# Kernel optimization log

Measured on AMD Instinct MI355X. Metric: run time of the kernel, lower is better.

Reference implementation:

```python
import jax, jax.numpy as jnp
import numpy as np

B, H = 16384, 1024  # batch, hidden (= input_size; module requires equality)


def _glorot(k, shape):
    lim = 1.0 / np.sqrt(shape[-1])
    return jax.random.uniform(k, shape, jnp.float32, -lim, lim)


def setup_inputs() -> dict:
    key = jax.random.key(0)
    ks = jax.random.split(key, 20)
    inp = {
        "d_t": jax.random.normal(ks[0], (B, H), jnp.float32),
        "h_t_minus_1": jax.random.normal(ks[1], (B, H), jnp.float32),
        "c_t_minus_1": jax.random.normal(ks[2], (B, H), jnp.float32),
    }
    names = ["i", "f", "o", "c", "g"]
    for n, (ka, kb, kc) in zip(names, zip(ks[3:8], ks[8:13], ks[13:18])):
        inp[f"W_{n}"] = _glorot(ka, (H, H))  # Linear weight [out,in], has bias
        inp[f"b_{n}"] = _glorot(kb, (H,))
        inp[f"U_{n}"] = _glorot(kc, (H, H))  # Linear weight, no bias
    return inp


def reference(d_t, h_t_minus_1, c_t_minus_1,
              W_i, b_i, U_i, W_f, b_f, U_f, W_o, b_o, U_o,
              W_c, b_c, U_c, W_g, b_g, U_g):
    def lin2(W, b, U):  # W(d) + U(h)
        return d_t @ W.T + b + h_t_minus_1 @ U.T

    i_t = jax.nn.sigmoid(lin2(W_i, b_i, U_i))
    f_t = jax.nn.sigmoid(lin2(W_f, b_f, U_f))
    o_t = jax.nn.sigmoid(lin2(W_o, b_o, U_o))
    c_hat_t = jnp.tanh(lin2(W_c, b_c, U_c))
    g_t = jax.nn.sigmoid(lin2(W_g, b_g, U_g))

    c_t = i_t * c_hat_t + f_t * c_t_minus_1
    # per-row dot products (original uses bmm on [B,1,H]x[B,H,1])
    num = jnp.sum(c_t * c_t_minus_1, axis=-1, keepdims=True)      # [B,1]
    den = jnp.sum(c_t_minus_1 * c_t_minus_1, axis=-1, keepdims=True)
    fraction = num / den                                           # [B,1] broadcast to [B,H]
    c_div_t = c_t - g_t * fraction * c_t_minus_1
    h_t = o_t * jnp.tanh(c_div_t)
    return (h_t, c_t)
```

## Files before the change

kernel.cpp:

```cpp
#include <hip/hip_runtime.h>
#include <hip/hip_bf16.h>

#define B_ROWS 16384
#define HDIM   1024
#define KDIM   2048
#define NDIM   5120

typedef __attribute__((ext_vector_type(8))) __bf16 bf16x8;
typedef __attribute__((ext_vector_type(4))) float  f32x4;

#define WS_OFF_B    67108864UL
#define WS_OFF_BIAS 88080384UL
#define WS_OFF_P    88100864UL

__device__ __forceinline__ void async16(const void* g, void* l) {
  __builtin_amdgcn_global_load_lds(
      (__attribute__((address_space(1))) void*)(g),
      (__attribute__((address_space(3))) void*)(l), 16, 0, 0);
}

__device__ __forceinline__ float fast_sigmoid(float x) {
  return 1.0f / (1.0f + __expf(-x));
}
__device__ __forceinline__ float fast_tanh(float x) {
  return 1.0f - 2.0f / (__expf(2.0f * x) + 1.0f);
}

struct GatePtrs {
  const float* W[5];
  const float* U[5];
  const float* b[5];
};

__global__ __launch_bounds__(256) void pack_A(const float* __restrict__ d,
                                              const float* __restrict__ h,
                                              __bf16* __restrict__ A) {
  const int idx = blockIdx.x * 256 + threadIdx.x;
  const size_t flat = (size_t)idx * 8;
  const int r = (int)(flat >> 11);
  const int c = (int)(flat & 2047);
  const float* src = (c < HDIM) ? (d + (size_t)r * HDIM + c)
                                : (h + (size_t)r * HDIM + (c - HDIM));
  const float4 v0 = ((const float4*)src)[0];
  const float4 v1 = ((const float4*)src)[1];
  bf16x8 o;
  o[0] = (__bf16)v0.x; o[1] = (__bf16)v0.y; o[2] = (__bf16)v0.z; o[3] = (__bf16)v0.w;
  o[4] = (__bf16)v1.x; o[5] = (__bf16)v1.y; o[6] = (__bf16)v1.z; o[7] = (__bf16)v1.w;
  *(bf16x8*)(A + flat) = o;
}

__global__ __launch_bounds__(256) void pack_B(GatePtrs gp, __bf16* __restrict__ Bm) {
  const int idx = blockIdx.x * 256 + threadIdx.x;
  const size_t flat = (size_t)idx * 8;
  const int row = (int)(flat >> 11);
  const int c = (int)(flat & 2047);
  const int g = row >> 10;
  const int oo = row & 1023;
  const float* base = (c < HDIM) ? gp.W[g] : gp.U[g];
  const float* src = base + (size_t)oo * HDIM + (c & 1023);
  const float4 v0 = ((const float4*)src)[0];
  const float4 v1 = ((const float4*)src)[1];
  bf16x8 o;
  o[0] = (__bf16)v0.x; o[1] = (__bf16)v0.y; o[2] = (__bf16)v0.z; o[3] = (__bf16)v0.w;
  o[4] = (__bf16)v1.x; o[5] = (__bf16)v1.y; o[6] = (__bf16)v1.z; o[7] = (__bf16)v1.w;
  *(bf16x8*)(Bm + flat) = o;
}

__global__ __launch_bounds__(256) void pack_bias(GatePtrs gp, float* __restrict__ bias) {
  const int i = blockIdx.x * 256 + threadIdx.x;
  bias[i] = gp.b[i >> 10][i & 1023];
}

__global__ __launch_bounds__(256) void gemm_act(const __bf16* __restrict__ A,
                                                const __bf16* __restrict__ Bm,
                                                const float* __restrict__ bias,
                                                __bf16* __restrict__ P) {
  __shared__ __align__(16) __bf16 As[128 * 64];
  __shared__ __align__(16) __bf16 Bs[128 * 64];

  const int tid  = threadIdx.x;
  const int lane = tid & 63;
  const int wave = tid >> 6;
  const int quad = lane >> 4;
  const int lr   = lane & 15;
  const int sx   = lr & 7;
  const int wm   = (wave >> 1) << 6;
  const int wn   = (wave & 1) << 6;

  const int row0 = blockIdx.x * 128;
  const int col0 = blockIdx.y * 128;

  f32x4 acc[4][4] = {};

  for (int kt = 0; kt < KDIM; kt += 64) {
#pragma unroll
    for (int t = 0; t < 4; ++t) {
      const int c  = t * 256 + tid;
      const int r  = c >> 3;
      const int q  = (c & 7) ^ (r & 7);
      async16(A  + (size_t)(row0 + r) * KDIM + kt + q * 8, As + c * 8);
      async16(Bm + (size_t)(col0 + r) * KDIM + kt + q * 8, Bs + c * 8);
    }
    __syncthreads();

#pragma unroll
    for (int kk = 0; kk < 64; kk += 32) {
      const int kq = (kk >> 3) + quad;
      bf16x8 af[4], bf[4];
#pragma unroll
      for (int i = 0; i < 4; ++i)
        af[i] = *(const bf16x8*)(As + (wm + i * 16 + lr) * 64 + ((kq ^ sx) << 3));
#pragma unroll
      for (int i = 0; i < 4; ++i)
        bf[i] = *(const bf16x8*)(Bs + (wn + i * 16 + lr) * 64 + ((kq ^ sx) << 3));
#pragma unroll
      for (int i = 0; i < 4; ++i)
#pragma unroll
        for (int j = 0; j < 4; ++j)
          acc[i][j] = __builtin_amdgcn_mfma_f32_16x16x32_bf16(af[i], bf[j], acc[i][j], 0, 0, 0);
    }
    __syncthreads();
  }

  const int gate = col0 >> 10;
#pragma unroll
  for (int i = 0; i < 4; ++i) {
    const int grow = row0 + wm + i * 16 + quad * 4;
#pragma unroll
    for (int j = 0; j < 4; ++j) {
      const int gcol = col0 + wn + j * 16 + lr;
      const float bv = bias[gcol];
#pragma unroll
      for (int r = 0; r < 4; ++r) {
        const float v = acc[i][j][r] + bv;
        const float a = (gate == 3) ? fast_tanh(v) : fast_sigmoid(v);
        P[(size_t)(grow + r) * NDIM + gcol] = (__bf16)a;
      }
    }
  }
}

__global__ __launch_bounds__(256) void fuse_out(const __bf16* __restrict__ P,
                                                const float* __restrict__ cprev,
                                                float* __restrict__ h_out,
                                                float* __restrict__ c_out) {
  const int r = blockIdx.x;
  const int t = threadIdx.x;
  const __bf16* Pr = P + (size_t)r * NDIM;
  const float* cpr = cprev + (size_t)r * HDIM;

  float ct[4], cp[4], ov[4], gv[4];
  float num = 0.f, den = 0.f;
#pragma unroll
  for (int q = 0; q < 4; ++q) {
    const int c = t + q * 256;
    const float iv = (float)Pr[c];
    const float fv = (float)Pr[HDIM + c];
    ov[q] = (float)Pr[2 * HDIM + c];
    const float ch = (float)Pr[3 * HDIM + c];
    gv[q] = (float)Pr[4 * HDIM + c];
    cp[q] = cpr[c];
    ct[q] = iv * ch + fv * cp[q];
    num += ct[q] * cp[q];
    den += cp[q] * cp[q];
  }
#pragma unroll
  for (int off = 32; off > 0; off >>= 1) {
    num += __shfl_down(num, off);
    den += __shfl_down(den, off);
  }
  __shared__ float sn[4], sd[4];
  const int lane = t & 63, wave = t >> 6;
  if (lane == 0) { sn[wave] = num; sd[wave] = den; }
  __syncthreads();
  const float frac = (sn[0] + sn[1] + sn[2] + sn[3]) /
                     (sd[0] + sd[1] + sd[2] + sd[3]);
#pragma unroll
  for (int q = 0; q < 4; ++q) {
    const int c = t + q * 256;
    const float cd = ct[q] - gv[q] * frac * cp[q];
    h_out[(size_t)r * HDIM + c] = ov[q] * fast_tanh(cd);
    c_out[(size_t)r * HDIM + c] = ct[q];
  }
}

extern "C" void kernel_launch(void* const* d_in, const int* in_sizes, int n_in,
                              void* d_out, int out_size, void* d_ws, size_t ws_size,
                              hipStream_t stream) {
  const float* d_t    = (const float*)d_in[0];
  const float* h_prev = (const float*)d_in[1];
  const float* c_prev = (const float*)d_in[2];
  GatePtrs gp;
  for (int g = 0; g < 5; ++g) {
    gp.W[g] = (const float*)d_in[3 + g * 3];
    gp.b[g] = (const float*)d_in[4 + g * 3];
    gp.U[g] = (const float*)d_in[5 + g * 3];
  }

  char* ws = (char*)d_ws;
  __bf16* Apack  = (__bf16*)ws;
  __bf16* Bpack  = (__bf16*)(ws + WS_OFF_B);
  float*  biasA  = (float*)(ws + WS_OFF_BIAS);
  __bf16* P      = (__bf16*)(ws + WS_OFF_P);

  float* h_out = (float*)d_out;
  float* c_out = h_out + (size_t)B_ROWS * HDIM;

  pack_A<<<dim3(B_ROWS * (KDIM / 2048)), 256, 0, stream>>>(d_t, h_prev, Apack);
  pack_B<<<dim3(NDIM), 256, 0, stream>>>(gp, Bpack);
  pack_bias<<<dim3(NDIM / 256), 256, 0, stream>>>(gp, biasA);
  gemm_act<<<dim3(B_ROWS / 128, NDIM / 128), 256, 0, stream>>>(Apack, Bpack, biasA, P);
  fuse_out<<<dim3(B_ROWS), 256, 0, stream>>>(P, c_prev, h_out, c_out);
}
```

Measured before the change: 801.6 us.

## Rewrite GEMM with 256x256 tiles, 4-stage async LDS pipeline and swizzled block order

The GEMM moves to 256x256 output tiles computed by 512 threads. Operands stream through a 4-deep LDS ring buffer filled by async global-to-LDS loads issued 3 k-steps ahead, with manual waitcnt/barrier control and setprio around the MFMA bursts. A block-index swizzle groups blocks for L2 reuse. The aim is to hide global load latency and raise arithmetic intensity, at the cost of more LDS use and fragile hand-written synchronisation.

Measured after the change: 724.7 us. 1.11x faster.

```diff
diff --git a/kernel.cpp b/kernel.cpp
--- a/kernel.cpp
+++ b/kernel.cpp
@@ -71,64 +71,103 @@
   bias[i] = gp.b[i >> 10][i & 1023];
 }
 
-__global__ __launch_bounds__(256) void gemm_act(const __bf16* __restrict__ A,
-                                                const __bf16* __restrict__ Bm,
-                                                const float* __restrict__ bias,
-                                                __bf16* __restrict__ P) {
-  __shared__ __align__(16) __bf16 As[128 * 64];
-  __shared__ __align__(16) __bf16 Bs[128 * 64];
+__global__ __launch_bounds__(512, 2) void gemm_act(const __bf16* __restrict__ A,
+                                                   const __bf16* __restrict__ Bm,
+                                                   const float* __restrict__ bias,
+                                                   __bf16* __restrict__ P) {
+  __shared__ __align__(16) __bf16 As[4][256 * 32];
+  __shared__ __align__(16) __bf16 Bs[4][256 * 32];
 
   const int tid  = threadIdx.x;
   const int lane = tid & 63;
   const int wave = tid >> 6;
   const int quad = lane >> 4;
   const int lr   = lane & 15;
-  const int sx   = lr & 7;
-  const int wm   = (wave >> 1) << 6;
-  const int wn   = (wave & 1) << 6;
-
-  const int row0 = blockIdx.x * 128;
-  const int col0 = blockIdx.y * 128;
-
-  f32x4 acc[4][4] = {};
-
-  for (int kt = 0; kt < KDIM; kt += 64) {
-#pragma unroll
-    for (int t = 0; t < 4; ++t) {
-      const int c  = t * 256 + tid;
-      const int r  = c >> 3;
-      const int q  = (c & 7) ^ (r & 7);
-      async16(A  + (size_t)(row0 + r) * KDIM + kt + q * 8, As + c * 8);
-      async16(Bm + (size_t)(col0 + r) * KDIM + kt + q * 8, Bs + c * 8);
+  const int wr   = wave >> 2;
+  const int wc   = wave & 3;
+  const int cOff = ((quad ^ ((lr >> 1) & 3)) << 3);
+
+  const int nb  = blockIdx.x;
+  const int sw  = (nb & 7) * 160 + (nb >> 3);
+  const int tm  = sw & 63;
+  const int tn  = sw >> 6;
+  const int row0 = tm << 8;
+  const int col0 = tn << 8;
+
+  const int c0 = tid, c1 = 512 + tid;
+  const __bf16* srcA0 = A  + (size_t)(row0 + (c0 >> 2)) * KDIM + (((c0 & 3) ^ ((c0 >> 3) & 3)) << 3);
+  const __bf16* srcA1 = A  + (size_t)(row0 + (c1 >> 2)) * KDIM + (((c1 & 3) ^ ((c1 >> 3) & 3)) << 3);
+  const __bf16* srcB0 = Bm + (size_t)(col0 + (c0 >> 2)) * KDIM + (((c0 & 3) ^ ((c0 >> 3) & 3)) << 3);
+  const __bf16* srcB1 = Bm + (size_t)(col0 + (c1 >> 2)) * KDIM + (((c1 & 3) ^ ((c1 >> 3) & 3)) << 3);
+
+  f32x4 acc[8][4] = {};
+
+  for (int kp = 0; kp < 3; ++kp) {
+    __bf16* da = As[kp];
+    __bf16* db = Bs[kp];
+    async16(srcA0 + kp * 32, da + (size_t)c0 * 8);
+    async16(srcA1 + kp * 32, da + (size_t)c1 * 8);
+    async16(srcB0 + kp * 32, db + (size_t)c0 * 8);
+    async16(srcB1 + kp * 32, db + (size_t)c1 * 8);
+  }
+  asm volatile("s_waitcnt vmcnt(8)" ::: "memory");
+  asm volatile("s_barrier" ::: "memory");
+
+  const int NT = KDIM / 32;
+  for (int k = 0; k < NT; ++k) {
+    const __bf16* ab = As[k & 3];
+    const __bf16* bb = Bs[k & 3];
+    const int kp = k + 3;
+    bf16x8 bf[4];
+#pragma unroll
+    for (int s = 0; s < 2; ++s) {
+      bf16x8 af[4];
+      if (s == 0) {
+#pragma unroll
+        for (int j = 0; j < 4; ++j)
+          bf[j] = *(const bf16x8*)(bb + (wc * 64 + j * 16 + lr) * 32 + cOff);
+      }
+#pragma unroll
+      for (int i = 0; i < 4; ++i)
+        af[i] = *(const bf16x8*)(ab + (wr * 128 + (s * 4 + i) * 16 + lr) * 32 + cOff);
+
+      if (kp < NT) {
+        if (s == 0) {
+          async16(srcA0 + kp * 32, As[kp & 3] + (size_t)c0 * 8);
+          async16(srcA1 + kp * 32, As[kp & 3] + (size_t)c1 * 8);
+        } else {
+          async16(srcB0 + kp * 32, Bs[kp & 3] + (size_t)c0 * 8);
+          async16(srcB1 + kp * 32, Bs[kp & 3] + (size_t)c1 * 8);
+        }
+      }
+
+      asm volatile("s_barrier" ::: "memory");
+      asm volatile("s_waitcnt lgkmcnt(0)" ::: "memory");
+      __builtin_amdgcn_s_setprio(1);
+#pragma unroll
+      for (int i = 0; i < 4; ++i)
+#pragma unroll
+        for (int j = 0; j < 4; ++j)
+          acc[s * 4 + i][j] =
+              __builtin_amdgcn_mfma_f32_16x16x32_bf16(af[i], bf[j], acc[s * 4 + i][j], 0, 0, 0);
+      __builtin_amdgcn_s_setprio(0);
+
+      if (s == 1) {
+        if (k < NT - 3)       { asm volatile("s_waitcnt vmcnt(8)" ::: "memory"); }
+        else if (k == NT - 3) { asm volatile("s_waitcnt vmcnt(4)" ::: "memory"); }
+        else if (k == NT - 2) { asm volatile("s_waitcnt vmcnt(0)" ::: "memory"); }
+      }
+      asm volatile("s_barrier" ::: "memory");
     }
-    __syncthreads();
-
-#pragma unroll
-    for (int kk = 0; kk < 64; kk += 32) {
-      const int kq = (kk >> 3) + quad;
-      bf16x8 af[4], bf[4];
-#pragma unroll
-      for (int i = 0; i < 4; ++i)
-        af[i] = *(const bf16x8*)(As + (wm + i * 16 + lr) * 64 + ((kq ^ sx) << 3));
-#pragma unroll
-      for (int i = 0; i < 4; ++i)
-        bf[i] = *(const bf16x8*)(Bs + (wn + i * 16 + lr) * 64 + ((kq ^ sx) << 3));
-#pragma unroll
-      for (int i = 0; i < 4; ++i)
-#pragma unroll
-        for (int j = 0; j < 4; ++j)
-          acc[i][j] = __builtin_amdgcn_mfma_f32_16x16x32_bf16(af[i], bf[j], acc[i][j], 0, 0, 0);
-    }
-    __syncthreads();
   }
 
   const int gate = col0 >> 10;
 #pragma unroll
-  for (int i = 0; i < 4; ++i) {
-    const int grow = row0 + wm + i * 16 + quad * 4;
+  for (int i = 0; i < 8; ++i) {
+    const int grow = row0 + wr * 128 + i * 16 + quad * 4;
 #pragma unroll
     for (int j = 0; j < 4; ++j) {
-      const int gcol = col0 + wn + j * 16 + lr;
+      const int gcol = col0 + wc * 64 + j * 16 + lr;
       const float bv = bias[gcol];
 #pragma unroll
       for (int r = 0; r < 4; ++r) {
@@ -209,6 +248,6 @@
   pack_A<<<dim3(B_ROWS * (KDIM / 2048)), 256, 0, stream>>>(d_t, h_prev, Apack);
   pack_B<<<dim3(NDIM), 256, 0, stream>>>(gp, Bpack);
   pack_bias<<<dim3(NDIM / 256), 256, 0, stream>>>(gp, biasA);
-  gemm_act<<<dim3(B_ROWS / 128, NDIM / 128), 256, 0, stream>>>(Apack, Bpack, biasA, P);
+  gemm_act<<<dim3((B_ROWS / 256) * (NDIM / 256)), 512, 0, stream>>>(Apack, Bpack, biasA, P);
   fuse_out<<<dim3(B_ROWS), 256, 0, stream>>>(P, c_prev, h_out, c_out);
 }
```

## Double-buffer GEMM with 128x256 tiles, 8 waves, swizzled grid, vectorized epilogue

Applied to the files above, without the earlier changes.

The GEMM kernel now uses 512 threads with a 128x256 output tile and a K-step of 32. Its LDS buffers are double-buffered so the next tile's global-to-LDS loads overlap the MFMA work on the current one, with raw barriers and s_setprio around the math. The grid is flattened and block indices are remapped so neighbouring blocks share A/B tiles in cache. The fuse_out kernel also switches to vectorized bf16x4/float4 loads and stores per thread. The aim is to hide memory latency and raise MFMA utilization, at the cost of more LDS per block and more fragile hand-written synchronization.

Result: faster. 708.8 us (-11.6%).

```diff
diff --git a/kernel.cpp b/kernel.cpp
--- a/kernel.cpp
+++ b/kernel.cpp
@@ -7,6 +7,7 @@
 #define NDIM   5120
 
 typedef __attribute__((ext_vector_type(8))) __bf16 bf16x8;
+typedef __attribute__((ext_vector_type(4))) __bf16 bf16x4;
 typedef __attribute__((ext_vector_type(4))) float  f32x4;
 
 #define WS_OFF_B    67108864UL
@@ -71,64 +72,89 @@
   bias[i] = gp.b[i >> 10][i & 1023];
 }
 
-__global__ __launch_bounds__(256) void gemm_act(const __bf16* __restrict__ A,
-                                                const __bf16* __restrict__ Bm,
-                                                const float* __restrict__ bias,
-                                                __bf16* __restrict__ P) {
-  __shared__ __align__(16) __bf16 As[128 * 64];
-  __shared__ __align__(16) __bf16 Bs[128 * 64];
+__global__ __launch_bounds__(512, 4) void gemm_act(const __bf16* __restrict__ A,
+                                                   const __bf16* __restrict__ Bm,
+                                                   const float* __restrict__ bias,
+                                                   __bf16* __restrict__ P) {
+  __shared__ __align__(16) __bf16 As[2][128 * 32];
+  __shared__ __align__(16) __bf16 Bs[2][256 * 32];
 
   const int tid  = threadIdx.x;
   const int lane = tid & 63;
   const int wave = tid >> 6;
   const int quad = lane >> 4;
   const int lr   = lane & 15;
-  const int sx   = lr & 7;
-  const int wm   = (wave >> 1) << 6;
-  const int wn   = (wave & 1) << 6;
-
-  const int row0 = blockIdx.x * 128;
-  const int col0 = blockIdx.y * 128;
+  const int wr   = wave >> 2;
+  const int wc   = wave & 3;
+  const int cOff = ((quad ^ ((lr >> 1) & 3)) << 3);
+
+  const int nb  = blockIdx.x;
+  const int sw  = (nb & 7) * 320 + (nb >> 3);
+  const int tm  = sw & 127;
+  const int tn  = sw >> 7;
+  const int row0 = tm << 7;
+  const int col0 = tn << 8;
+
+  const int swz = (((tid & 3) ^ ((tid >> 3) & 3)) << 3);
+  const __bf16* srcA = A  + (size_t)(row0 + (tid >> 2)) * KDIM + swz;
+  const __bf16* srcB = Bm + (size_t)(col0 + (tid >> 2)) * KDIM + swz;
+  const size_t bOff2 = (size_t)128 * KDIM;
 
   f32x4 acc[4][4] = {};
 
-  for (int kt = 0; kt < KDIM; kt += 64) {
-#pragma unroll
-    for (int t = 0; t < 4; ++t) {
-      const int c  = t * 256 + tid;
-      const int r  = c >> 3;
-      const int q  = (c & 7) ^ (r & 7);
-      async16(A  + (size_t)(row0 + r) * KDIM + kt + q * 8, As + c * 8);
-      async16(Bm + (size_t)(col0 + r) * KDIM + kt + q * 8, Bs + c * 8);
+  async16(srcA,         As[0] + (size_t)tid * 8);
+  async16(srcB,         Bs[0] + (size_t)tid * 8);
+  async16(srcB + bOff2, Bs[0] + (size_t)tid * 8 + 4096);
+  asm volatile("s_waitcnt vmcnt(0)" ::: "memory");
+  asm volatile("s_barrier" ::: "memory");
+
+  const int NT = KDIM / 32;
+  for (int k = 0; k < NT; ++k) {
+    const __bf16* ab = As[k & 1];
+    const __bf16* bb = Bs[k & 1];
+    const bool pf = (k + 1) < NT;
+
+    bf16x8 af[4], bf[4];
+#pragma unroll
+    for (int i = 0; i < 4; ++i)
+      af[i] = *(const bf16x8*)(ab + (wr * 64 + i * 16 + lr) * 32 + cOff);
+#pragma unroll
+    for (int j = 0; j < 4; ++j)
+      bf[j] = *(const bf16x8*)(bb + (wc * 64 + j * 16 + lr) * 32 + cOff);
+
+    if (pf) {
+      const int kc = (k + 1) * 32;
+      __bf16* da = As[(k + 1) & 1];
+      __bf16* db = Bs[(k + 1) & 1];
+      async16(srcA + kc,         da + (size_t)tid * 8);
+      async16(srcB + kc,         db + (size_t)tid * 8);
+      async16(srcB + bOff2 + kc, db + (size_t)tid * 8 + 4096);
     }
-    __syncthreads();
-
-#pragma unroll
-    for (int kk = 0; kk < 64; kk += 32) {
-      const int kq = (kk >> 3) + quad;
-      bf16x8 af[4], bf[4];
-#pragma unroll
-      for (int i = 0; i < 4; ++i)
-        af[i] = *(const bf16x8*)(As + (wm + i * 16 + lr) * 64 + ((kq ^ sx) << 3));
-#pragma unroll
-      for (int i = 0; i < 4; ++i)
-        bf[i] = *(const bf16x8*)(Bs + (wn + i * 16 + lr) * 64 + ((kq ^ sx) << 3));
-#pragma unroll
-      for (int i = 0; i < 4; ++i)
-#pragma unroll
-        for (int j = 0; j < 4; ++j)
-          acc[i][j] = __builtin_amdgcn_mfma_f32_16x16x32_bf16(af[i], bf[j], acc[i][j], 0, 0, 0);
+
+    asm volatile("s_barrier" ::: "memory");
+    asm volatile("s_waitcnt lgkmcnt(0)" ::: "memory");
+    __builtin_amdgcn_s_setprio(1);
+#pragma unroll
+    for (int i = 0; i < 4; ++i)
+#pragma unroll
+      for (int j = 0; j < 4; ++j)
+        acc[i][j] =
+            __builtin_amdgcn_mfma_f32_16x16x32_bf16(af[i], bf[j], acc[i][j], 0, 0, 0);
+    __builtin_amdgcn_s_setprio(0);
+
+    if (pf) {
+      asm volatile("s_waitcnt vmcnt(0)" ::: "memory");
     }
-    __syncthreads();
+    asm volatile("s_barrier" ::: "memory");
   }
 
   const int gate = col0 >> 10;
 #pragma unroll
   for (int i = 0; i < 4; ++i) {
-    const int grow = row0 + wm + i * 16 + quad * 4;
+    const int grow = row0 + wr * 64 + i * 16 + quad * 4;
 #pragma unroll
     for (int j = 0; j < 4; ++j) {
-      const int gcol = col0 + wn + j * 16 + lr;
+      const int gcol = col0 + wc * 64 + j * 16 + lr;
       const float bv = bias[gcol];
 #pragma unroll
       for (int r = 0; r < 4; ++r) {
@@ -148,19 +174,21 @@
   const int t = threadIdx.x;
   const __bf16* Pr = P + (size_t)r * NDIM;
   const float* cpr = cprev + (size_t)r * HDIM;
-
-  float ct[4], cp[4], ov[4], gv[4];
+  const int c0 = t * 4;
+
+  const bf16x4 iv = *(const bf16x4*)(Pr + c0);
+  const bf16x4 fv = *(const bf16x4*)(Pr + HDIM + c0);
+  const bf16x4 ov = *(const bf16x4*)(Pr + 2 * HDIM + c0);
+  const bf16x4 ch = *(const bf16x4*)(Pr + 3 * HDIM + c0);
+  const bf16x4 gv = *(const bf16x4*)(Pr + 4 * HDIM + c0);
+  const float4 cp4 = *(const float4*)(cpr + c0);
+  const float cp[4] = {cp4.x, cp4.y, cp4.z, cp4.w};
+
+  float ct[4];
   float num = 0.f, den = 0.f;
 #pragma unroll
   for (int q = 0; q < 4; ++q) {
-    const int c = t + q * 256;
-    const float iv = (float)Pr[c];
-    const float fv = (float)Pr[HDIM + c];
-    ov[q] = (float)Pr[2 * HDIM + c];
-    const float ch = (float)Pr[3 * HDIM + c];
-    gv[q] = (float)Pr[4 * HDIM + c];
-    cp[q] = cpr[c];
-    ct[q] = iv * ch + fv * cp[q];
+    ct[q] = (float)iv[q] * (float)ch[q] + (float)fv[q] * cp[q];
     num += ct[q] * cp[q];
     den += cp[q] * cp[q];
   }
@@ -175,13 +203,18 @@
   __syncthreads();
   const float frac = (sn[0] + sn[1] + sn[2] + sn[3]) /
                      (sd[0] + sd[1] + sd[2] + sd[3]);
+
+  float4 ho, co;
+  float hv[4];
 #pragma unroll
   for (int q = 0; q < 4; ++q) {
-    const int c = t + q * 256;
-    const float cd = ct[q] - gv[q] * frac * cp[q];
-    h_out[(size_t)r * HDIM + c] = ov[q] * fast_tanh(cd);
-    c_out[(size_t)r * HDIM + c] = ct[q];
-  }
+    const float cd = ct[q] - (float)gv[q] * frac * cp[q];
+    hv[q] = (float)ov[q] * fast_tanh(cd);
+  }
+  ho.x = hv[0]; ho.y = hv[1]; ho.z = hv[2]; ho.w = hv[3];
+  co.x = ct[0]; co.y = ct[1]; co.z = ct[2]; co.w = ct[3];
+  *(float4*)(h_out + (size_t)r * HDIM + c0) = ho;
+  *(float4*)(c_out + (size_t)r * HDIM + c0) = co;
 }
 
 extern "C" void kernel_launch(void* const* d_in, const int* in_sizes, int n_in,
@@ -209,6 +242,6 @@
   pack_A<<<dim3(B_ROWS * (KDIM / 2048)), 256, 0, stream>>>(d_t, h_prev, Apack);
   pack_B<<<dim3(NDIM), 256, 0, stream>>>(gp, Bpack);
   pack_bias<<<dim3(NDIM / 256), 256, 0, stream>>>(gp, biasA);
-  gemm_act<<<dim3(B_ROWS / 128, NDIM / 128), 256, 0, stream>>>(Apack, Bpack, biasA, P);
+  gemm_act<<<dim3((B_ROWS / 128) * (NDIM / 256)), 512, 0, stream>>>(Apack, Bpack, biasA, P);
   fuse_out<<<dim3(B_ROWS), 256, 0, stream>>>(P, c_prev, h_out, c_out);
 }
```
